# Kernel tuning notes

Measured on AMD Instinct MI355X. Metric: run time of the kernel, lower is better.

The kernel has to match this reference:

```python
import jax, jax.numpy as jnp
import numpy as np

N = 50000      # nodes
E = 800000     # edges (avg degree 16)
D_IN = 128
D_H = 128
D_OUT = 64
SLOPE = 0.2    # leaky-relu negative slope (from the 0.2 constants in the graph)


def setup_inputs() -> dict:
    key = jax.random.key(0)
    ks = jax.random.split(key, 18)
    def w(k, shape, fan_in):
        return jax.random.normal(k, shape, jnp.float32) / np.sqrt(fan_in)
    inp = {
        "x": jax.random.normal(ks[0], (N, D_IN), jnp.float32),
        "W0": w(ks[1], (D_IN, D_H), D_IN),
        "b0": jnp.zeros((D_H,), jnp.float32),
        "Wq1": w(ks[2], (D_H, D_H), D_H),
        "bq1": jnp.zeros((D_H,), jnp.float32),
        "Wp1": w(ks[3], (D_H, D_H), D_H),
        "bp1": jnp.zeros((D_H,), jnp.float32),
        "a1": 0.1 * w(ks[4], (D_H,), D_H),
        "bg2": jnp.zeros((D_H,), jnp.float32),
        "Wq2": w(ks[5], (D_H, D_OUT), D_H),
        "bq2": jnp.zeros((D_OUT,), jnp.float32),
        "Wp2": w(ks[6], (D_H, D_OUT), D_H),
        "bp2": jnp.zeros((D_OUT,), jnp.float32),
        "a2": 0.1 * w(ks[7], (D_OUT,), D_OUT),
        "b_out": jnp.zeros((D_OUT,), jnp.float32),
        "src": jax.random.randint(ks[8], (E,), 0, N),
        "dst": jax.random.randint(ks[9], (E,), 0, N),
        "num_nodes": N,
    }
    return inp


def _gat_block(m, src, dst, Wq, bq, Wp, bp, a, n):
    # m: [N, d_in]; q/p: [N, d]
    q = m @ Wq + bq
    p = m @ Wp + bp
    # edge scores: s_e = sum_d leaky_relu(q[dst_e] + p[src_e]) * a_d   [E]
    e = jax.nn.leaky_relu(q[dst] + p[src], SLOPE)          # [E, d]
    s = jnp.einsum("ed,d->e", e, a)                        # [E]
    es = jnp.exp(s)                                        # unstabilized exp, as in source graph
    denom = jax.ops.segment_sum(es, dst, num_segments=n)   # [N]
    alpha = es / denom[dst]                                # [E] edge softmax over incoming edges
    # aggregate messages alpha_e * p[src_e] into dst nodes
    agg = jax.ops.segment_sum(alpha[:, None] * p[src], dst, num_segments=n)  # [N, d]
    return agg


def reference(x, W0, b0, Wq1, bq1, Wp1, bp1, a1, bg2, Wq2, bq2, Wp2, bp2, a2, b_out, src, dst, num_nodes):
    m1 = jax.nn.gelu(x @ W0 + b0, approximate=False)       # erf GELU per graph constants
    h1 = _gat_block(m1, src, dst, Wq1, bq1, Wp1, bp1, a1, num_nodes)
    m2 = jax.nn.gelu(h1 + bg2, approximate=False)
    h2 = _gat_block(m2, src, dst, Wq2, bq2, Wp2, bp2, a2, num_nodes)
    return h2 + b_out
```

## Files before the change

### kernel.cpp

```cpp
#include <hip/hip_runtime.h>
#include <hip/hip_bf16.h>
#include <math.h>


#define SLOPE 0.2f

typedef __attribute__((ext_vector_type(8))) __bf16 bf16x8;
typedef __attribute__((ext_vector_type(4))) float f32x4;

__device__ __forceinline__ float gelu_erf(float x) {
    return 0.5f * x * (1.0f + erff(x * 0.70710678118654752f));
}

__device__ __forceinline__ unsigned short f2bf(float f) {
    unsigned int u = __float_as_uint(f);
    return (unsigned short)((u + 0x7fffu + ((u >> 16) & 1u)) >> 16);
}
__device__ __forceinline__ float bf2f(unsigned short h) {
    return __uint_as_float((unsigned int)h << 16);
}

__device__ __forceinline__ float row16_sum(float x) {
    x += __int_as_float(__builtin_amdgcn_update_dpp(0, __float_as_int(x), 0x121, 0xF, 0xF, true));
    x += __int_as_float(__builtin_amdgcn_update_dpp(0, __float_as_int(x), 0x122, 0xF, 0xF, true));
    x += __int_as_float(__builtin_amdgcn_update_dpp(0, __float_as_int(x), 0x124, 0xF, 0xF, true));
    x += __int_as_float(__builtin_amdgcn_update_dpp(0, __float_as_int(x), 0x128, 0xF, 0xF, true));
    return x;
}

__device__ __forceinline__ int swz(int off) { return off ^ ((off >> 4) & 0x70); }

__global__ __launch_bounds__(256) void pack_w(
    const float* __restrict__ W0,  const float* __restrict__ Wq1,
    const float* __restrict__ Wp1, const float* __restrict__ Wq2,
    const float* __restrict__ Wp2,
    unsigned short* __restrict__ P0,  unsigned short* __restrict__ Pq1,
    unsigned short* __restrict__ Pp1, unsigned short* __restrict__ Pq2,
    unsigned short* __restrict__ Pp2)
{
    const float* W; unsigned short* P; int C;
    switch (blockIdx.y) {
        case 0:  W = W0;  P = P0;  C = 128; break;
        case 1:  W = Wq1; P = Pq1; C = 128; break;
        case 2:  W = Wp1; P = Pp1; C = 128; break;
        case 3:  W = Wq2; P = Pq2; C = 64;  break;
        default: W = Wp2; P = Pp2; C = 64;  break;
    }
    int i = blockIdx.x * 256 + threadIdx.x;
    int CE = C * 128;
    if (i >= CE) return;
    int j = i & 7, l = (i >> 3) & 63, ks = (i >> 9) & 3, ct = i >> 11;
    int k = ks * 32 + ((l >> 4) << 3) + j;
    int n = ct * 16 + (l & 15);
    float v = W[k * C + n];
    unsigned short hb = f2bf(v);
    P[i] = hb;
    P[CE + i] = f2bf(v - bf2f(hb));
}

__global__ __launch_bounds__(256) void gemm_fused01(
    const float* __restrict__ x,
    const unsigned short* __restrict__ P0,  const float* __restrict__ b0,
    const unsigned short* __restrict__ Pq1, const float* __restrict__ bq1,
    const unsigned short* __restrict__ Pp1, const float* __restrict__ bp1,
    float* __restrict__ outq, unsigned short* __restrict__ outp, int N)
{
    constexpr int CE = 128 * 128;
    __shared__ __align__(16) unsigned char lds[32768];

    const int t = threadIdx.x;
    const int lane = t & 63;
    const int w = t >> 6;
    const int row0 = blockIdx.x * 64;
    const int mcol = lane & 15;
    const int hk = lane >> 4;

    bf16x8 w1h[2][4], w1l[2][4];
#pragma unroll
    for (int c = 0; c < 2; c++)
#pragma unroll
        for (int ks = 0; ks < 4; ks++) {
            const unsigned short* Wp = P0 + (((w * 2 + c) * 4 + ks) * 64 + lane) * 8;
            w1h[c][ks] = *reinterpret_cast<const bf16x8*>(Wp);
            w1l[c][ks] = *reinterpret_cast<const bf16x8*>(Wp + CE);
        }

#pragma unroll
    for (int i = 0; i < 8; i++) {
        int idx = t + i * 256;
        int row = idx >> 5;
        int gr = row0 + row;
        float4 v = make_float4(0.f, 0.f, 0.f, 0.f);
        if (gr < N) v = *reinterpret_cast<const float4*>(x + (size_t)gr * 128 + (idx & 31) * 4);
        const float* f = reinterpret_cast<const float*>(&v);
        unsigned int h[4], l[4];
#pragma unroll
        for (int j = 0; j < 4; j++) {
            unsigned short hb = f2bf(f[j]);
            h[j] = hb;
            l[j] = f2bf(f[j] - bf2f(hb));
        }
        int so = swz(row * 256 + (idx & 31) * 8);
        *reinterpret_cast<uint2*>(&lds[so])         = make_uint2(h[0] | (h[1] << 16), h[2] | (h[3] << 16));
        *reinterpret_cast<uint2*>(&lds[16384 + so]) = make_uint2(l[0] | (l[1] << 16), l[2] | (l[3] << 16));
    }
    __syncthreads();

    f32x4 acc1[2][4];
#pragma unroll
    for (int c = 0; c < 2; c++)
#pragma unroll
        for (int rf = 0; rf < 4; rf++) acc1[c][rf] = (f32x4){0.f, 0.f, 0.f, 0.f};

#pragma unroll
    for (int ks = 0; ks < 4; ks++) {
        bf16x8 ah[4], al[4];
#pragma unroll
        for (int rf = 0; rf < 4; rf++) {
            int so = swz((rf * 16 + mcol) * 256 + ks * 64 + hk * 16);
            ah[rf] = *reinterpret_cast<const bf16x8*>(&lds[so]);
            al[rf] = *reinterpret_cast<const bf16x8*>(&lds[16384 + so]);
        }
#pragma unroll
        for (int c = 0; c < 2; c++) {
#pragma unroll
            for (int rf = 0; rf < 4; rf++) {
                acc1[c][rf] = __builtin_amdgcn_mfma_f32_16x16x32_bf16(ah[rf], w1h[c][ks], acc1[c][rf], 0, 0, 0);
                acc1[c][rf] = __builtin_amdgcn_mfma_f32_16x16x32_bf16(al[rf], w1h[c][ks], acc1[c][rf], 0, 0, 0);
                acc1[c][rf] = __builtin_amdgcn_mfma_f32_16x16x32_bf16(ah[rf], w1l[c][ks], acc1[c][rf], 0, 0, 0);
            }
        }
    }
    __syncthreads();

    bf16x8 w2h[2][4], w2l[2][4];
#pragma unroll
    for (int c = 0; c < 2; c++)
#pragma unroll
        for (int ks = 0; ks < 4; ks++) {
            const unsigned short* Wp = Pq1 + (((w * 2 + c) * 4 + ks) * 64 + lane) * 8;
            w2h[c][ks] = *reinterpret_cast<const bf16x8*>(Wp);
            w2l[c][ks] = *reinterpret_cast<const bf16x8*>(Wp + CE);
        }

#pragma unroll
    for (int c = 0; c < 2; c++) {
        int col = (w * 2 + c) * 16 + mcol;
        float bv = b0[col];
#pragma unroll
        for (int rf = 0; rf < 4; rf++) {
#pragma unroll
            for (int r = 0; r < 4; r++) {
                int row = rf * 16 + hk * 4 + r;
                float v = gelu_erf(acc1[c][rf][r] + bv);
                unsigned short hb = f2bf(v);
                int bo = row * 256 + col * 2;
                *reinterpret_cast<unsigned short*>(&lds[swz(bo)])         = hb;
                *reinterpret_cast<unsigned short*>(&lds[16384 + swz(bo)]) = f2bf(v - bf2f(hb));
            }
        }
    }
    __syncthreads();

    f32x4 acc2[2][4];
#pragma unroll
    for (int c = 0; c < 2; c++)
#pragma unroll
        for (int rf = 0; rf < 4; rf++) acc2[c][rf] = (f32x4){0.f, 0.f, 0.f, 0.f};

#pragma unroll
    for (int ks = 0; ks < 4; ks++) {
        bf16x8 ah[4], al[4];
#pragma unroll
        for (int rf = 0; rf < 4; rf++) {
            int so = swz((rf * 16 + mcol) * 256 + ks * 64 + hk * 16);
            ah[rf] = *reinterpret_cast<const bf16x8*>(&lds[so]);
            al[rf] = *reinterpret_cast<const bf16x8*>(&lds[16384 + so]);
        }
#pragma unroll
        for (int c = 0; c < 2; c++) {
#pragma unroll
            for (int rf = 0; rf < 4; rf++) {
                acc2[c][rf] = __builtin_amdgcn_mfma_f32_16x16x32_bf16(ah[rf], w2h[c][ks], acc2[c][rf], 0, 0, 0);
                acc2[c][rf] = __builtin_amdgcn_mfma_f32_16x16x32_bf16(al[rf], w2h[c][ks], acc2[c][rf], 0, 0, 0);
                acc2[c][rf] = __builtin_amdgcn_mfma_f32_16x16x32_bf16(ah[rf], w2l[c][ks], acc2[c][rf], 0, 0, 0);
            }
        }
    }

    bf16x8 w3h[2][4], w3l[2][4];
#pragma unroll
    for (int c = 0; c < 2; c++)
#pragma unroll
        for (int ks = 0; ks < 4; ks++) {
            const unsigned short* Wp = Pp1 + (((w * 2 + c) * 4 + ks) * 64 + lane) * 8;
            w3h[c][ks] = *reinterpret_cast<const bf16x8*>(Wp);
            w3l[c][ks] = *reinterpret_cast<const bf16x8*>(Wp + CE);
        }

#pragma unroll
    for (int c = 0; c < 2; c++) {
        int col = (w * 2 + c) * 16 + mcol;
        float bv = bq1[col];
#pragma unroll
        for (int rf = 0; rf < 4; rf++) {
#pragma unroll
            for (int r = 0; r < 4; r++) {
                int row = rf * 16 + hk * 4 + r;
                int gr = row0 + row;
                if (gr < N) outq[(size_t)gr * 128 + col] = acc2[c][rf][r] + bv;
            }
        }
    }

#pragma unroll
    for (int c = 0; c < 2; c++)
#pragma unroll
        for (int rf = 0; rf < 4; rf++) acc2[c][rf] = (f32x4){0.f, 0.f, 0.f, 0.f};

#pragma unroll
    for (int ks = 0; ks < 4; ks++) {
        bf16x8 ah[4], al[4];
#pragma unroll
        for (int rf = 0; rf < 4; rf++) {
            int so = swz((rf * 16 + mcol) * 256 + ks * 64 + hk * 16);
            ah[rf] = *reinterpret_cast<const bf16x8*>(&lds[so]);
            al[rf] = *reinterpret_cast<const bf16x8*>(&lds[16384 + so]);
        }
#pragma unroll
        for (int c = 0; c < 2; c++) {
#pragma unroll
            for (int rf = 0; rf < 4; rf++) {
                acc2[c][rf] = __builtin_amdgcn_mfma_f32_16x16x32_bf16(ah[rf], w3h[c][ks], acc2[c][rf], 0, 0, 0);
                acc2[c][rf] = __builtin_amdgcn_mfma_f32_16x16x32_bf16(al[rf], w3h[c][ks], acc2[c][rf], 0, 0, 0);
                acc2[c][rf] = __builtin_amdgcn_mfma_f32_16x16x32_bf16(ah[rf], w3l[c][ks], acc2[c][rf], 0, 0, 0);
            }
        }
    }
    __syncthreads();

#pragma unroll
    for (int c = 0; c < 2; c++) {
        int col = (w * 2 + c) * 16 + mcol;
        float bv = bp1[col];
#pragma unroll
        for (int rf = 0; rf < 4; rf++) {
#pragma unroll
            for (int r = 0; r < 4; r++) {
                int row = rf * 16 + hk * 4 + r;
                *reinterpret_cast<unsigned short*>(&lds[swz(row * 256 + col * 2)]) =
                    f2bf(acc2[c][rf][r] + bv);
            }
        }
    }
    __syncthreads();
#pragma unroll
    for (int i = 0; i < 4; i++) {
        int idx = t + i * 256;
        int row = idx >> 4;
        int sl = idx & 15;
        int gr = row0 + row;
        if (gr < N)
            *reinterpret_cast<uint4*>(outp + (size_t)gr * 128 + sl * 8) =
                *reinterpret_cast<const uint4*>(&lds[swz(row * 256 + sl * 16)]);
    }
}

__global__ __launch_bounds__(256) void mfma_gemm64(
    const unsigned short* __restrict__ AHg, const unsigned short* __restrict__ ALg,
    const unsigned short* __restrict__ P1, const float* __restrict__ b1,
    const unsigned short* __restrict__ P2, const float* __restrict__ b2,
    float* __restrict__ outq, unsigned short* __restrict__ outp, int N)
{
    constexpr int CE = 64 * 128;
    __shared__ __align__(16) unsigned char lds[32768];

    const int t = threadIdx.x;
    const int lane = t & 63;
    const int w = t >> 6;
    const int row0 = blockIdx.x * 64;
    const int mcol = lane & 15;
    const int hk = lane >> 4;

    bf16x8 wh[2][4], wl[2][4];
#pragma unroll
    for (int c = 0; c < 2; c++)
#pragma unroll
        for (int ks = 0; ks < 4; ks++) {
            int ctg = w * 2 + c;
            bool isq = ctg < 4;
            int ct = isq ? ctg : ctg - 4;
            const unsigned short* Wp = (isq ? P1 : P2) + ((ct * 4 + ks) * 64 + lane) * 8;
            wh[c][ks] = *reinterpret_cast<const bf16x8*>(Wp);
            wl[c][ks] = *reinterpret_cast<const bf16x8*>(Wp + CE);
        }

#pragma unroll
    for (int i = 0; i < 4; i++) {
        int idx = t + i * 256;
        int row = idx >> 4;
        int gr = row0 + row;
        uint4 vh = make_uint4(0, 0, 0, 0), vl = make_uint4(0, 0, 0, 0);
        if (gr < N) {
            vh = *reinterpret_cast<const uint4*>(AHg + (size_t)gr * 128 + (idx & 15) * 8);
            vl = *reinterpret_cast<const uint4*>(ALg + (size_t)gr * 128 + (idx & 15) * 8);
        }
        int so = swz(row * 256 + (idx & 15) * 16);
        *reinterpret_cast<uint4*>(&lds[so])         = vh;
        *reinterpret_cast<uint4*>(&lds[16384 + so]) = vl;
    }
    __syncthreads();

    f32x4 acc[2][4];
#pragma unroll
    for (int c = 0; c < 2; c++)
#pragma unroll
        for (int rf = 0; rf < 4; rf++) acc[c][rf] = (f32x4){0.f, 0.f, 0.f, 0.f};

#pragma unroll
    for (int ks = 0; ks < 4; ks++) {
        bf16x8 ah[4], al[4];
#pragma unroll
        for (int rf = 0; rf < 4; rf++) {
            int so = swz((rf * 16 + mcol) * 256 + ks * 64 + hk * 16);
            ah[rf] = *reinterpret_cast<const bf16x8*>(&lds[so]);
            al[rf] = *reinterpret_cast<const bf16x8*>(&lds[16384 + so]);
        }
#pragma unroll
        for (int c = 0; c < 2; c++) {
#pragma unroll
            for (int rf = 0; rf < 4; rf++) {
                acc[c][rf] = __builtin_amdgcn_mfma_f32_16x16x32_bf16(ah[rf], wh[c][ks], acc[c][rf], 0, 0, 0);
                acc[c][rf] = __builtin_amdgcn_mfma_f32_16x16x32_bf16(al[rf], wh[c][ks], acc[c][rf], 0, 0, 0);
                acc[c][rf] = __builtin_amdgcn_mfma_f32_16x16x32_bf16(ah[rf], wl[c][ks], acc[c][rf], 0, 0, 0);
            }
        }
    }
    __syncthreads();

#pragma unroll
    for (int c = 0; c < 2; c++) {
        int ctg = w * 2 + c;
        bool isq = ctg < 4;
        int ct = isq ? ctg : ctg - 4;
        int col = ct * 16 + mcol;
        float bv = (isq ? b1 : b2)[col];
#pragma unroll
        for (int rf = 0; rf < 4; rf++) {
#pragma unroll
            for (int r = 0; r < 4; r++) {
                int row = rf * 16 + hk * 4 + r;
                int gr = row0 + row;
                float v = acc[c][rf][r] + bv;
                if (isq) {
                    if (gr < N) outq[(size_t)gr * 64 + col] = v;
                } else {
                    *reinterpret_cast<unsigned short*>(&lds[swz(row * 256 + col * 2)]) = f2bf(v);
                }
            }
        }
    }
    __syncthreads();
#pragma unroll
    for (int i = 0; i < 2; i++) {
        int idx = t + i * 256;
        int row = idx >> 3;
        int sl = idx & 7;
        int gr = row0 + row;
        if (gr < N)
            *reinterpret_cast<uint4*>(outp + (size_t)gr * 64 + sl * 8) =
                *reinterpret_cast<const uint4*>(&lds[swz(row * 256 + sl * 16)]);
    }
}


__global__ __launch_bounds__(256) void hist_coarse(
    const int* __restrict__ dst, int* __restrict__ gh, int E, int CB)
{
    __shared__ int cnt[4096];
    const int blk = blockIdx.x;
    const int t = threadIdx.x;
    for (int b = t; b < CB; b += 256) cnt[b] = 0;
    __syncthreads();
    const int epb = (E + 63) / 64;
    const int s = blk * epb;
    const int e_ = (s + epb < E) ? s + epb : E;
    for (int i = s + t; i < e_; i += 256)
        atomicAdd(&cnt[dst[i] >> 4], 1);
    __syncthreads();
    for (int b = t; b < CB; b += 256)
        gh[b * 64 + blk] = cnt[b];
}

__global__ __launch_bounds__(256) void scan1_kernel(const int* __restrict__ gh,
                                                    int* __restrict__ gscan,
                                                    int* __restrict__ bsum, int M)
{
    __shared__ int lds[256];
    int t = threadIdx.x;
    int i = blockIdx.x * 256 + t;
    int v = (i < M) ? gh[i] : 0;
    lds[t] = v;
    __syncthreads();
    int x = v;
    for (int off = 1; off < 256; off <<= 1) {
        int y = (t >= off) ? lds[t - off] : 0;
        __syncthreads();
        x += y;
        lds[t] = x;
        __syncthreads();
    }
    if (i < M) gscan[i] = x - v;
    if (t == 255) bsum[blockIdx.x] = x;
}

__global__ __launch_bounds__(1024) void scan2_kernel(int* __restrict__ bsum, int NB)
{
    __shared__ int lds[1024];
    int t = threadIdx.x;
    int v = (t < NB) ? bsum[t] : 0;
    lds[t] = v;
    __syncthreads();
    int x = v;
    for (int off = 1; off < 1024; off <<= 1) {
        int y = (t >= off) ? lds[t - off] : 0;
        __syncthreads();
        x += y;
        lds[t] = x;
        __syncthreads();
    }
    if (t < NB) bsum[t] = x - v;
}

__global__ __launch_bounds__(256) void scan3_kernel(int* __restrict__ gscan,
                                                    const int* __restrict__ bsum, int M)
{
    int i = blockIdx.x * 256 + threadIdx.x;
    if (i < M) gscan[i] += bsum[blockIdx.x];
}

__global__ __launch_bounds__(256) void scatter_coarse(
    const int* __restrict__ src, const int* __restrict__ dst,
    const int* __restrict__ gscan, int2* __restrict__ pairs, int E, int CB)
{
    __shared__ int cur[4096];
    const int blk = blockIdx.x;
    const int t = threadIdx.x;
    for (int b = t; b < CB; b += 256)
        cur[b] = gscan[b * 64 + blk];
    __syncthreads();
    const int epb = (E + 63) / 64;
    const int s = blk * epb;
    const int e_ = (s + epb < E) ? s + epb : E;
    for (int i = s + t; i < e_; i += 256) {
        int d = dst[i];
        int sv = src[i];
        int pos = atomicAdd(&cur[d >> 4], 1);
        pairs[pos] = make_int2(d, sv);
    }
}

__global__ __launch_bounds__(256) void finalize_kernel(
    const int2* __restrict__ pairs, const int* __restrict__ gscan,
    int* __restrict__ offs, int* __restrict__ csr_src, int N, int E, int CB)
{
    const int wid = blockIdx.x * 4 + (threadIdx.x >> 6);
    const int lane = threadIdx.x & 63;
    if (wid >= CB) return;

    const int s    = gscan[wid * 64];
    const int e_   = (wid + 1 < CB) ? gscan[(wid + 1) * 64] : E;
    const int base = wid * 16;
    const unsigned long long ltmask = (lane == 63) ? ~0ull >> 1
                                                   : (1ull << lane) - 1ull;

    int rc[16];
#pragma unroll
    for (int j = 0; j < 16; j++) rc[j] = 0;
    for (int c0 = s; c0 < e_; c0 += 64) {
        int i = c0 + lane;
        int d = (i < e_) ? pairs[i].x - base : -1;
#pragma unroll
        for (int j = 0; j < 16; j++)
            rc[j] += (int)__popcll(__ballot(d == j));
    }

    int pref[16];
    int run = s;
#pragma unroll
    for (int j = 0; j < 16; j++) { pref[j] = run; run += rc[j]; }
    int pref_v = 0;
#pragma unroll
    for (int j = 0; j < 16; j++) pref_v = (lane == j) ? pref[j] : pref_v;

    if (lane < 16 && base + lane < N) offs[base + lane] = pref_v;
    if (wid == CB - 1 && lane == 16) offs[N] = E;

    int rcv = 0;
    for (int c0 = s; c0 < e_; c0 += 64) {
        int i = c0 + lane;
        const bool act = i < e_;
        int2 pr = act ? pairs[i] : make_int2(base - 1, 0);
        int d = pr.x - base;
        unsigned long long msel = 0;
        int addcnt = 0;
#pragma unroll
        for (int j = 0; j < 16; j++) {
            unsigned long long m = __ballot(d == j);
            if (d == j) msel = m;
            if (lane == j) addcnt = (int)__popcll(m);
        }
        int subrank = (int)__popcll(msel & ltmask);
        int posbase = __builtin_amdgcn_ds_bpermute(d * 4, pref_v + rcv);
        if (act) csr_src[posbase + subrank] = pr.y;
        rcv += addcnt;
    }
}

template <int D, int EPI>
__global__ __launch_bounds__(256) void gat_agg(
    const float* __restrict__ q, const unsigned short* __restrict__ p,
    const float* __restrict__ a, const float* __restrict__ bvec,
    const int* __restrict__ offs, const int* __restrict__ csr_src,
    float* __restrict__ out, unsigned short* __restrict__ mhi,
    unsigned short* __restrict__ mlo, int N)
{
    constexpr int VPL = D / 16;
    const int t = threadIdx.x;
    const int lane = t & 63;
    const int sl = lane & 15;
    const int base = sl * VPL;
    const int node = blockIdx.x * 16 + ((t >> 6) << 2) + (lane >> 4);
    const bool valid = node < N;

    float qv[VPL], a6[VPL], a4[VPL], acc[VPL];
#pragma unroll
    for (int v = 0; v < VPL; v++) { qv[v] = 0.f; acc[v] = 0.f; }
    if (valid) {
        const float* qp = q + (size_t)node * D + base;
        float4 q0 = *reinterpret_cast<const float4*>(qp);
        qv[0] = q0.x; qv[1] = q0.y; qv[2] = q0.z; qv[3] = q0.w;
        if constexpr (VPL == 8) {
            float4 q1 = *reinterpret_cast<const float4*>(qp + 4);
            qv[4] = q1.x; qv[5] = q1.y; qv[6] = q1.z; qv[7] = q1.w;
        }
    }
#pragma unroll
    for (int v = 0; v < VPL; v++) {
        float av = a[base + v];
        a6[v] = 0.6f * av;
        a4[v] = 0.4f * av;
    }

    auto gather = [&](int s) -> uint4 {
        if constexpr (D == 128) {
            return *reinterpret_cast<const uint4*>(p + (size_t)s * 128 + base);
        } else {
            uint2 u = *reinterpret_cast<const uint2*>(p + (size_t)s * 64 + base);
            return make_uint4(u.x, u.y, 0u, 0u);
        }
    };
    auto unpack = [&](uint4 u, float* pv) {
        pv[0] = __uint_as_float(u.x << 16); pv[1] = __uint_as_float(u.x & 0xffff0000u);
        pv[2] = __uint_as_float(u.y << 16); pv[3] = __uint_as_float(u.y & 0xffff0000u);
        if constexpr (VPL == 8) {
            pv[4] = __uint_as_float(u.z << 16); pv[5] = __uint_as_float(u.z & 0xffff0000u);
            pv[6] = __uint_as_float(u.w << 16); pv[7] = __uint_as_float(u.w & 0xffff0000u);
        }
    };

    float denom = 0.f;
    int e  = valid ? offs[node] : 0;
    int e1 = valid ? offs[node + 1] : 0;

    int s0 = csr_src[(e + 0 < e1) ? e + 0 : 0];
    int s1 = csr_src[(e + 1 < e1) ? e + 1 : 0];
    int s2 = csr_src[(e + 2 < e1) ? e + 2 : 0];
    int s3 = csr_src[(e + 3 < e1) ? e + 3 : 0];
    uint4 uA0 = gather(s0), uA1 = gather(s1), uA2 = gather(s2), uA3 = gather(s3);
    int en = e + 4;
    int n0 = csr_src[(en + 0 < e1) ? en + 0 : 0];
    int n1 = csr_src[(en + 1 < e1) ? en + 1 : 0];
    int n2 = csr_src[(en + 2 < e1) ? en + 2 : 0];
    int n3 = csr_src[(en + 3 < e1) ? en + 3 : 0];

    while (__any(e < e1)) {
        const bool a0 = (e + 0) < e1, a1b = (e + 1) < e1,
                   a2 = (e + 2) < e1, a3 = (e + 3) < e1;

        uint4 v0 = gather(n0), v1 = gather(n1), v2 = gather(n2), v3 = gather(n3);

        const int em = en + 4;
        const int m0 = csr_src[(em + 0 < e1) ? em + 0 : 0];
        const int m1 = csr_src[(em + 1 < e1) ? em + 1 : 0];
        const int m2 = csr_src[(em + 2 < e1) ? em + 2 : 0];
        const int m3 = csr_src[(em + 3 < e1) ? em + 3 : 0];

        float pv[4][VPL];
        unpack(uA0, pv[0]); unpack(uA1, pv[1]); unpack(uA2, pv[2]); unpack(uA3, pv[3]);

        float pa0 = 0.f, pa1 = 0.f, pa2 = 0.f, pa3 = 0.f;
#pragma unroll
        for (int v = 0; v < VPL; v++) {
            float d0 = qv[v] + pv[0][v];
            float d1 = qv[v] + pv[1][v];
            float d2 = qv[v] + pv[2][v];
            float d3 = qv[v] + pv[3][v];
            pa0 = fmaf(d0, a6[v], pa0); pa0 = fmaf(fabsf(d0), a4[v], pa0);
            pa1 = fmaf(d1, a6[v], pa1); pa1 = fmaf(fabsf(d1), a4[v], pa1);
            pa2 = fmaf(d2, a6[v], pa2); pa2 = fmaf(fabsf(d2), a4[v], pa2);
            pa3 = fmaf(d3, a6[v], pa3); pa3 = fmaf(fabsf(d3), a4[v], pa3);
        }

        float r0 = row16_sum(pa0);
        float r1 = row16_sum(pa1);
        float r2 = row16_sum(pa2);
        float r3 = row16_sum(pa3);

        float esm0 = a0  ? __expf(r0) : 0.f;
        float esm1 = a1b ? __expf(r1) : 0.f;
        float esm2 = a2  ? __expf(r2) : 0.f;
        float esm3 = a3  ? __expf(r3) : 0.f;
        denom += (esm0 + esm1) + (esm2 + esm3);
#pragma unroll
        for (int v = 0; v < VPL; v++) {
            acc[v] = fmaf(esm0, pv[0][v], acc[v]);
            acc[v] = fmaf(esm1, pv[1][v], acc[v]);
            acc[v] = fmaf(esm2, pv[2][v], acc[v]);
            acc[v] = fmaf(esm3, pv[3][v], acc[v]);
        }

        uA0 = v0; uA1 = v1; uA2 = v2; uA3 = v3;
        n0 = m0; n1 = m1; n2 = m2; n3 = m3;
        e = en; en = em;
    }

    if (!valid) return;
    float inv = (denom != 0.f) ? 1.f / denom : 0.f;
    if constexpr (EPI == 0) {
        union { unsigned short us[8]; uint4 v; } H, L;
#pragma unroll
        for (int v = 0; v < VPL; v++) {
            float g = gelu_erf(acc[v] * inv + bvec[base + v]);
            H.us[v] = f2bf(g);
            L.us[v] = f2bf(g - bf2f(H.us[v]));
        }
        *reinterpret_cast<uint4*>(mhi + (size_t)node * 128 + base) = H.v;
        *reinterpret_cast<uint4*>(mlo + (size_t)node * 128 + base) = L.v;
    } else {
        union { float f[4]; float4 v; } O;
#pragma unroll
        for (int v = 0; v < VPL; v++) O.f[v] = acc[v] * inv + bvec[base + v];
        *reinterpret_cast<float4*>(out + (size_t)node * D + base) = O.v;
    }
}

extern "C" void kernel_launch(void* const* d_in, const int* in_sizes, int n_in,
                              void* d_out, int out_size, void* d_ws, size_t ws_size,
                              hipStream_t stream)
{
    const float* x     = (const float*)d_in[0];
    const float* W0    = (const float*)d_in[1];
    const float* b0    = (const float*)d_in[2];
    const float* Wq1   = (const float*)d_in[3];
    const float* bq1   = (const float*)d_in[4];
    const float* Wp1   = (const float*)d_in[5];
    const float* bp1   = (const float*)d_in[6];
    const float* a1    = (const float*)d_in[7];
    const float* bg2   = (const float*)d_in[8];
    const float* Wq2   = (const float*)d_in[9];
    const float* bq2   = (const float*)d_in[10];
    const float* Wp2   = (const float*)d_in[11];
    const float* bp2   = (const float*)d_in[12];
    const float* a2    = (const float*)d_in[13];
    const float* b_out = (const float*)d_in[14];
    const int*   src   = (const int*)d_in[15];
    const int*   dst   = (const int*)d_in[16];

    const int N = in_sizes[0] / 128;
    const int E = in_sizes[15];
    float* out = (float*)d_out;

    float* q_buf        = (float*)d_ws;
    unsigned short* pb  = (unsigned short*)(q_buf + (size_t)N * 128);
    unsigned short* Mhi = pb + (size_t)N * 128;
    unsigned short* Mlo = Mhi + (size_t)N * 128;
    unsigned short* P0  = Mlo + (size_t)N * 128;
    unsigned short* Pq1 = P0  + 128 * 128 * 2;
    unsigned short* Pp1 = Pq1 + 128 * 128 * 2;
    unsigned short* Pq2 = Pp1 + 128 * 128 * 2;
    unsigned short* Pp2 = Pq2 + 128 * 64 * 2;
    int* offs    = (int*)(Pp2 + 128 * 64 * 2);
    int* csr_src = offs + (N + 2);
    const int CB = (N + 15) / 16;
    const int M  = CB * 64;
    int* gh    = csr_src + E;
    int* gscan = gh + M;
    int* bsum  = gscan + M;
    int2* pairs = (int2*)q_buf;

    const int NB1 = (M + 255) / 256;

    pack_w<<<dim3(64, 5), 256, 0, stream>>>(W0, Wq1, Wp1, Wq2, Wp2,
                                            P0, Pq1, Pp1, Pq2, Pp2);
    hist_coarse<<<64, 256, 0, stream>>>(dst, gh, E, CB);
    scan1_kernel<<<NB1, 256, 0, stream>>>(gh, gscan, bsum, M);
    scan2_kernel<<<1, 1024, 0, stream>>>(bsum, NB1);
    scan3_kernel<<<NB1, 256, 0, stream>>>(gscan, bsum, M);
    scatter_coarse<<<64, 256, 0, stream>>>(src, dst, gscan, pairs, E, CB);
    finalize_kernel<<<(CB + 3) / 4, 256, 0, stream>>>(pairs, gscan, offs, csr_src, N, E, CB);

    const int GB64 = (N + 63) / 64;
    const int GGAT = (N + 15) / 16;

    gemm_fused01<<<GB64, 256, 0, stream>>>(
        x, P0, b0, Pq1, bq1, Pp1, bp1, q_buf, pb, N);
    gat_agg<128, 0><<<GGAT, 256, 0, stream>>>(
        q_buf, pb, a1, bg2, offs, csr_src,
        nullptr, Mhi, Mlo, N);
    mfma_gemm64<<<GB64, 256, 0, stream>>>(
        Mhi, Mlo, Pq2, bq2, Pp2, bp2,
        q_buf, pb, N);
    gat_agg<64, 1><<<GGAT, 256, 0, stream>>>(
        q_buf, pb, a2, b_out, offs, csr_src,
        out, nullptr, nullptr, N);
}
```

Measured before the change: 283.4 us.

## Fuse CSR build and weight packing into one cooperative grid-synced kernel

```diff
diff --git a/kernel.cpp b/kernel.cpp
--- a/kernel.cpp
+++ b/kernel.cpp
@@ -1,6 +1,9 @@
 #include <hip/hip_runtime.h>
 #include <hip/hip_bf16.h>
+#include <hip/hip_cooperative_groups.h>
 #include <math.h>
+
+namespace cg = cooperative_groups;
 
 
 #define SLOPE 0.2f
@@ -29,34 +32,6 @@
 }
 
 __device__ __forceinline__ int swz(int off) { return off ^ ((off >> 4) & 0x70); }
-
-__global__ __launch_bounds__(256) void pack_w(
-    const float* __restrict__ W0,  const float* __restrict__ Wq1,
-    const float* __restrict__ Wp1, const float* __restrict__ Wq2,
-    const float* __restrict__ Wp2,
-    unsigned short* __restrict__ P0,  unsigned short* __restrict__ Pq1,
-    unsigned short* __restrict__ Pp1, unsigned short* __restrict__ Pq2,
-    unsigned short* __restrict__ Pp2)
-{
-    const float* W; unsigned short* P; int C;
-    switch (blockIdx.y) {
-        case 0:  W = W0;  P = P0;  C = 128; break;
-        case 1:  W = Wq1; P = Pq1; C = 128; break;
-        case 2:  W = Wp1; P = Pp1; C = 128; break;
-        case 3:  W = Wq2; P = Pq2; C = 64;  break;
-        default: W = Wp2; P = Pp2; C = 64;  break;
-    }
-    int i = blockIdx.x * 256 + threadIdx.x;
-    int CE = C * 128;
-    if (i >= CE) return;
-    int j = i & 7, l = (i >> 3) & 63, ks = (i >> 9) & 3, ct = i >> 11;
-    int k = ks * 32 + ((l >> 4) << 3) + j;
-    int n = ct * 16 + (l & 15);
-    float v = W[k * C + n];
-    unsigned short hb = f2bf(v);
-    P[i] = hb;
-    P[CE + i] = f2bf(v - bf2f(hb));
-}
 
 __global__ __launch_bounds__(256) void gemm_fused01(
     const float* __restrict__ x,
@@ -373,147 +348,185 @@
     }
 }
 
-
-__global__ __launch_bounds__(256) void hist_coarse(
-    const int* __restrict__ dst, int* __restrict__ gh, int E, int CB)
+__global__ __launch_bounds__(256) void csr_build(
+    const float* __restrict__ W0,  const float* __restrict__ Wq1,
+    const float* __restrict__ Wp1, const float* __restrict__ Wq2,
+    const float* __restrict__ Wp2,
+    unsigned short* __restrict__ P0,  unsigned short* __restrict__ Pq1,
+    unsigned short* __restrict__ Pp1, unsigned short* __restrict__ Pq2,
+    unsigned short* __restrict__ Pp2,
+    const int* __restrict__ src, const int* __restrict__ dst,
+    int* __restrict__ gh, int* __restrict__ gscan, int* __restrict__ bsum,
+    int2* __restrict__ pairs, int* __restrict__ offs, int* __restrict__ csr_src,
+    int N, int E, int CB)
 {
-    __shared__ int cnt[4096];
+    cg::grid_group grid = cg::this_grid();
+    __shared__ int smem[4096];
     const int blk = blockIdx.x;
+    const int NB = gridDim.x;
     const int t = threadIdx.x;
-    for (int b = t; b < CB; b += 256) cnt[b] = 0;
-    __syncthreads();
-    const int epb = (E + 63) / 64;
-    const int s = blk * epb;
-    const int e_ = (s + epb < E) ? s + epb : E;
-    for (int i = s + t; i < e_; i += 256)
-        atomicAdd(&cnt[dst[i] >> 4], 1);
-    __syncthreads();
-    for (int b = t; b < CB; b += 256)
-        gh[b * 64 + blk] = cnt[b];
-}
-
-__global__ __launch_bounds__(256) void scan1_kernel(const int* __restrict__ gh,
-                                                    int* __restrict__ gscan,
-                                                    int* __restrict__ bsum, int M)
-{
-    __shared__ int lds[256];
-    int t = threadIdx.x;
-    int i = blockIdx.x * 256 + t;
-    int v = (i < M) ? gh[i] : 0;
-    lds[t] = v;
+    const int lane = t & 63;
+    const int M = CB * 64;
+
+    if (blk < 64) {
+        for (int b = t; b < CB; b += 256) smem[b] = 0;
+        __syncthreads();
+        const int epb = (E + 63) / 64;
+        const int s = blk * epb;
+        const int e_ = (s + epb < E) ? s + epb : E;
+        for (int i = s + t; i < e_; i += 256)
+            atomicAdd(&smem[dst[i] >> 4], 1);
+        __syncthreads();
+        for (int b = t; b < CB; b += 256)
+            gh[b * 64 + blk] = smem[b];
+    } else if (blk < 384) {
+        const int pbi = blk - 64;
+        const int mat = pbi >> 6;
+        const int ib  = pbi & 63;
+        const float* W; unsigned short* P; int C;
+        switch (mat) {
+            case 0:  W = W0;  P = P0;  C = 128; break;
+            case 1:  W = Wq1; P = Pq1; C = 128; break;
+            case 2:  W = Wp1; P = Pp1; C = 128; break;
+            case 3:  W = Wq2; P = Pq2; C = 64;  break;
+            default: W = Wp2; P = Pp2; C = 64;  break;
+        }
+        int i = ib * 256 + t;
+        int CE = C * 128;
+        if (i < CE) {
+            int j = i & 7, l = (i >> 3) & 63, ks = (i >> 9) & 3, ct = i >> 11;
+            int k = ks * 32 + ((l >> 4) << 3) + j;
+            int n = ct * 16 + (l & 15);
+            float v = W[k * C + n];
+            unsigned short hb = f2bf(v);
+            P[i] = hb;
+            P[CE + i] = f2bf(v - bf2f(hb));
+        }
+    }
+    __threadfence();
+    grid.sync();
+
+    const int gi = blk * 256 + t;
+    const int v = (gi < M) ? gh[gi] : 0;
+    __syncthreads();
+    smem[t] = v;
     __syncthreads();
     int x = v;
     for (int off = 1; off < 256; off <<= 1) {
-        int y = (t >= off) ? lds[t - off] : 0;
+        int y = (t >= off) ? smem[t - off] : 0;
         __syncthreads();
         x += y;
-        lds[t] = x;
+        smem[t] = x;
         __syncthreads();
     }
-    if (i < M) gscan[i] = x - v;
-    if (t == 255) bsum[blockIdx.x] = x;
-}
-
-__global__ __launch_bounds__(1024) void scan2_kernel(int* __restrict__ bsum, int NB)
-{
-    __shared__ int lds[1024];
-    int t = threadIdx.x;
-    int v = (t < NB) ? bsum[t] : 0;
-    lds[t] = v;
-    __syncthreads();
-    int x = v;
-    for (int off = 1; off < 1024; off <<= 1) {
-        int y = (t >= off) ? lds[t - off] : 0;
+    const int local_excl = x - v;
+    if (t == 255) bsum[blk] = x;
+    __threadfence();
+    grid.sync();
+
+    if (blk == 0) {
+        int vals[4];
+        int tsum = 0;
+        const int base = t * 4;
+#pragma unroll
+        for (int j = 0; j < 4; j++) {
+            int idx = base + j;
+            int bv = (idx < NB) ? bsum[idx] : 0;
+            vals[j] = tsum;
+            tsum += bv;
+        }
         __syncthreads();
-        x += y;
-        lds[t] = x;
+        smem[t] = tsum;
         __syncthreads();
-    }
-    if (t < NB) bsum[t] = x - v;
-}
-
-__global__ __launch_bounds__(256) void scan3_kernel(int* __restrict__ gscan,
-                                                    const int* __restrict__ bsum, int M)
-{
-    int i = blockIdx.x * 256 + threadIdx.x;
-    if (i < M) gscan[i] += bsum[blockIdx.x];
-}
-
-__global__ __launch_bounds__(256) void scatter_coarse(
-    const int* __restrict__ src, const int* __restrict__ dst,
-    const int* __restrict__ gscan, int2* __restrict__ pairs, int E, int CB)
-{
-    __shared__ int cur[4096];
-    const int blk = blockIdx.x;
-    const int t = threadIdx.x;
-    for (int b = t; b < CB; b += 256)
-        cur[b] = gscan[b * 64 + blk];
-    __syncthreads();
-    const int epb = (E + 63) / 64;
-    const int s = blk * epb;
-    const int e_ = (s + epb < E) ? s + epb : E;
-    for (int i = s + t; i < e_; i += 256) {
-        int d = dst[i];
-        int sv = src[i];
-        int pos = atomicAdd(&cur[d >> 4], 1);
-        pairs[pos] = make_int2(d, sv);
-    }
-}
-
-__global__ __launch_bounds__(256) void finalize_kernel(
-    const int2* __restrict__ pairs, const int* __restrict__ gscan,
-    int* __restrict__ offs, int* __restrict__ csr_src, int N, int E, int CB)
-{
-    const int wid = blockIdx.x * 4 + (threadIdx.x >> 6);
-    const int lane = threadIdx.x & 63;
-    if (wid >= CB) return;
-
-    const int s    = gscan[wid * 64];
-    const int e_   = (wid + 1 < CB) ? gscan[(wid + 1) * 64] : E;
-    const int base = wid * 16;
-    const unsigned long long ltmask = (lane == 63) ? ~0ull >> 1
-                                                   : (1ull << lane) - 1ull;
-
-    int rc[16];
-#pragma unroll
-    for (int j = 0; j < 16; j++) rc[j] = 0;
-    for (int c0 = s; c0 < e_; c0 += 64) {
-        int i = c0 + lane;
-        int d = (i < e_) ? pairs[i].x - base : -1;
-#pragma unroll
-        for (int j = 0; j < 16; j++)
-            rc[j] += (int)__popcll(__ballot(d == j));
-    }
-
-    int pref[16];
-    int run = s;
-#pragma unroll
-    for (int j = 0; j < 16; j++) { pref[j] = run; run += rc[j]; }
-    int pref_v = 0;
-#pragma unroll
-    for (int j = 0; j < 16; j++) pref_v = (lane == j) ? pref[j] : pref_v;
-
-    if (lane < 16 && base + lane < N) offs[base + lane] = pref_v;
-    if (wid == CB - 1 && lane == 16) offs[N] = E;
-
-    int rcv = 0;
-    for (int c0 = s; c0 < e_; c0 += 64) {
-        int i = c0 + lane;
-        const bool act = i < e_;
-        int2 pr = act ? pairs[i] : make_int2(base - 1, 0);
-        int d = pr.x - base;
-        unsigned long long msel = 0;
-        int addcnt = 0;
-#pragma unroll
-        for (int j = 0; j < 16; j++) {
-            unsigned long long m = __ballot(d == j);
-            if (d == j) msel = m;
-            if (lane == j) addcnt = (int)__popcll(m);
-        }
-        int subrank = (int)__popcll(msel & ltmask);
-        int posbase = __builtin_amdgcn_ds_bpermute(d * 4, pref_v + rcv);
-        if (act) csr_src[posbase + subrank] = pr.y;
-        rcv += addcnt;
+        int xx = tsum;
+        for (int off = 1; off < 256; off <<= 1) {
+            int y = (t >= off) ? smem[t - off] : 0;
+            __syncthreads();
+            xx += y;
+            smem[t] = xx;
+            __syncthreads();
+        }
+        const int tpref = xx - tsum;
+#pragma unroll
+        for (int j = 0; j < 4; j++) {
+            int idx = base + j;
+            if (idx < NB) bsum[idx] = tpref + vals[j];
+        }
+        __threadfence();
+    }
+    grid.sync();
+
+    if (gi < M) gscan[gi] = bsum[blk] + local_excl;
+    __threadfence();
+    grid.sync();
+
+    if (blk < 64) {
+        __syncthreads();
+        for (int b = t; b < CB; b += 256)
+            smem[b] = gscan[b * 64 + blk];
+        __syncthreads();
+        const int epb = (E + 63) / 64;
+        const int s = blk * epb;
+        const int e_ = (s + epb < E) ? s + epb : E;
+        for (int i = s + t; i < e_; i += 256) {
+            int d = dst[i];
+            int sv = src[i];
+            int pos = atomicAdd(&smem[d >> 4], 1);
+            pairs[pos] = make_int2(d, sv);
+        }
+    }
+    __threadfence();
+    grid.sync();
+
+    const int wid = blk * 4 + (t >> 6);
+    if (wid < CB) {
+        const int s    = gscan[wid * 64];
+        const int e_   = (wid + 1 < CB) ? gscan[(wid + 1) * 64] : E;
+        const int base = wid * 16;
+        const unsigned long long ltmask = (lane == 63) ? ~0ull >> 1
+                                                       : (1ull << lane) - 1ull;
+
+        int rc[16];
+#pragma unroll
+        for (int j = 0; j < 16; j++) rc[j] = 0;
+        for (int c0 = s; c0 < e_; c0 += 64) {
+            int i = c0 + lane;
+            int d = (i < e_) ? pairs[i].x - base : -1;
+#pragma unroll
+            for (int j = 0; j < 16; j++)
+                rc[j] += (int)__popcll(__ballot(d == j));
+        }
+
+        int pref[16];
+        int run = s;
+#pragma unroll
+        for (int j = 0; j < 16; j++) { pref[j] = run; run += rc[j]; }
+        int pref_v = 0;
+#pragma unroll
+        for (int j = 0; j < 16; j++) pref_v = (lane == j) ? pref[j] : pref_v;
+
+        if (lane < 16 && base + lane < N) offs[base + lane] = pref_v;
+        if (wid == CB - 1 && lane == 16) offs[N] = E;
+
+        int rcv = 0;
+        for (int c0 = s; c0 < e_; c0 += 64) {
+            int i = c0 + lane;
+            const bool act = i < e_;
+            int2 pr = act ? pairs[i] : make_int2(base - 1, 0);
+            int d = pr.x - base;
+            unsigned long long msel = 0;
+            int addcnt = 0;
+#pragma unroll
+            for (int j = 0; j < 16; j++) {
+                unsigned long long m = __ballot(d == j);
+                if (d == j) msel = m;
+                if (lane == j) addcnt = (int)__popcll(m);
+            }
+            int subrank = (int)__popcll(msel & ltmask);
+            int posbase = __builtin_amdgcn_ds_bpermute(d * 4, pref_v + rcv);
+            if (act) csr_src[posbase + subrank] = pr.y;
+            rcv += addcnt;
+        }
     }
 }
 
@@ -699,16 +712,21 @@
     int* bsum  = gscan + M;
     int2* pairs = (int2*)q_buf;
 
-    const int NB1 = (M + 255) / 256;
-
-    pack_w<<<dim3(64, 5), 256, 0, stream>>>(W0, Wq1, Wp1, Wq2, Wp2,
-                                            P0, Pq1, Pp1, Pq2, Pp2);
-    hist_coarse<<<64, 256, 0, stream>>>(dst, gh, E, CB);
-    scan1_kernel<<<NB1, 256, 0, stream>>>(gh, gscan, bsum, M);
-    scan2_kernel<<<1, 1024, 0, stream>>>(bsum, NB1);
-    scan3_kernel<<<NB1, 256, 0, stream>>>(gscan, bsum, M);
-    scatter_coarse<<<64, 256, 0, stream>>>(src, dst, gscan, pairs, E, CB);
-    finalize_kernel<<<(CB + 3) / 4, 256, 0, stream>>>(pairs, gscan, offs, csr_src, N, E, CB);
+    int NB = (M + 255) / 256;
+    if (NB < 384) NB = 384;
+
+    {
+        void* args[] = {
+            (void*)&W0, (void*)&Wq1, (void*)&Wp1, (void*)&Wq2, (void*)&Wp2,
+            (void*)&P0, (void*)&Pq1, (void*)&Pp1, (void*)&Pq2, (void*)&Pp2,
+            (void*)&src, (void*)&dst,
+            (void*)&gh, (void*)&gscan, (void*)&bsum,
+            (void*)&pairs, (void*)&offs, (void*)&csr_src,
+            (void*)&N, (void*)&E, (void*)&CB
+        };
+        hipLaunchCooperativeKernel((const void*)csr_build, dim3(NB), dim3(256),
+                                   args, 0, stream);
+    }
 
     const int GB64 = (N + 63) / 64;
     const int GGAT = (N + 15) / 16;
```

After: 903.7 us. 3.19x slower.
